# Kernel optimization log

Measured on AMD Instinct MI355X. Metric: run time of the kernel, lower is better.

Reference implementation:

```python
import jax, jax.numpy as jnp
import numpy as np

EPS = 1e-5
GROUPS = 32


def _groupnorm(x, gamma, beta):
    B, C, H, W = x.shape
    xr = x.reshape(B, GROUPS, C // GROUPS, H, W)
    mu = xr.mean(axis=(2, 3, 4), keepdims=True)
    var = xr.var(axis=(2, 3, 4), keepdims=True)
    xn = ((xr - mu) * jax.lax.rsqrt(var + EPS)).reshape(B, C, H, W)
    return xn * gamma[None, :, None, None] + beta[None, :, None, None]


def _conv1x1(x, w, b):
    # x: [B,C,H,W], w: [Cout,Cin], b: [Cout]
    return jnp.einsum('bchw,oc->bohw', x, w) + b[None, :, None, None]


def setup_inputs() -> dict:
    key = jax.random.key(0)
    ks = jax.random.split(key, 11)
    B, C, H, W = 4, 64, 64, 64
    s = 0.05  # weight scale for well-conditioned softmax
    inp = {
        'x': jax.random.normal(ks[0], (B, C, H, W), jnp.float32),
        'gn_gamma': jnp.ones((C,), jnp.float32),
        'gn_beta': jnp.zeros((C,), jnp.float32),
        'wq': jax.random.normal(ks[1], (C, C), jnp.float32) * s,
        'bq': jnp.zeros((C,), jnp.float32),
        'wk': jax.random.normal(ks[2], (C, C), jnp.float32) * s,
        'bk': jnp.zeros((C,), jnp.float32),
        'wv': jax.random.normal(ks[3], (C, C), jnp.float32) * s,
        'bv': jnp.zeros((C,), jnp.float32),
        'wp': jax.random.normal(ks[4], (C, C), jnp.float32) * s,
        'bp': jnp.zeros((C,), jnp.float32),
    }
    return inp


def reference(x, gn_gamma, gn_beta, wq, bq, wk, bk, wv, bv, wp, bp):
    B, C, H, W = x.shape
    h = _groupnorm(x, gn_gamma, gn_beta)
    q = _conv1x1(h, wq, bq)
    k = _conv1x1(h, wk, bk)
    v = _conv1x1(h, wv, bv)
    # scores over all spatial positions: [B,H,W,H,W]
    scale = 1.0 / jnp.sqrt(jnp.asarray(C, x.dtype))
    w = jnp.einsum('bchw,bcHW->bhwHW', q, k) * scale
    w = jax.nn.softmax(w.reshape(B, H, W, H * W), axis=-1).reshape(B, H, W, H, W)
    h = jnp.einsum('bhwHW,bcHW->bchw', w, v)
    h = _conv1x1(h, wp, bp)
    return x + h
```

## Files before the change

### kernel.cpp

```cpp
#include <hip/hip_runtime.h>
#include <stdint.h>

#define Bn 4
#define Cn 64
#define Sn 4096
#define Gn 32

typedef float v4f __attribute__((ext_vector_type(4)));
typedef short v8s __attribute__((ext_vector_type(8)));
typedef short v4s __attribute__((ext_vector_type(4)));

#define MFMA16(a,b,c) __builtin_amdgcn_mfma_f32_16x16x32_bf16((a),(b),(c),0,0,0)

__device__ __forceinline__ float bf2f(uint16_t u){
  union { uint32_t i; float f; } x; x.i = ((uint32_t)u) << 16; return x.f;
}
__device__ __forceinline__ uint16_t f2bf(float f){
  union { float f; uint32_t i; } x; x.f = f;
  uint32_t r = x.i + 0x7fffu + ((x.i >> 16) & 1u);
  return (uint16_t)(r >> 16);
}
__device__ __forceinline__ uint32_t cvtpk(float a, float b){
  uint32_t r;
  asm("v_cvt_pk_bf16_f32 %0, %1, %2" : "=v"(r) : "v"(a), "v"(b));
  return r;
}
__device__ __forceinline__ v8s pack8(float4 a, float4 b){
  v8s r;
  r[0]=(short)f2bf(a.x); r[1]=(short)f2bf(a.y); r[2]=(short)f2bf(a.z); r[3]=(short)f2bf(a.w);
  r[4]=(short)f2bf(b.x); r[5]=(short)f2bf(b.y); r[6]=(short)f2bf(b.z); r[7]=(short)f2bf(b.w);
  return r;
}

__global__ __launch_bounds__(256) void gn_stats(const float* __restrict__ x,
                                                float* __restrict__ stats)
{
  const int tid = threadIdx.x;
  const float* base = x + (size_t)blockIdx.x * 8192;
  float sum = 0.f, sq = 0.f;
  #pragma unroll
  for (int i = 0; i < 8; ++i) {
    float4 v = *(const float4*)(base + ((i << 8) + tid)*4);
    sum += v.x + v.y + v.z + v.w;
    sq  += v.x*v.x + v.y*v.y + v.z*v.z + v.w*v.w;
  }
  #pragma unroll
  for (int off = 1; off < 64; off <<= 1) {
    sum += __shfl_xor(sum, off);
    sq  += __shfl_xor(sq, off);
  }
  __shared__ float red[8];
  const int w = tid >> 6;
  if ((tid & 63) == 0) { red[w] = sum; red[4+w] = sq; }
  __syncthreads();
  if (tid == 0) {
    float s = red[0]+red[1]+red[2]+red[3];
    float q = red[4]+red[5]+red[6]+red[7];
    float mean = s * (1.f/8192.f);
    float var  = q * (1.f/8192.f) - mean*mean;
    stats[blockIdx.x]       = mean;
    stats[128 + blockIdx.x] = rsqrtf(fmaxf(var, 0.f) + 1e-5f);
  }
}

__global__ __launch_bounds__(256) void gn_qkv(
    const float* __restrict__ xg, const float* __restrict__ gamma,
    const float* __restrict__ beta,
    const float* __restrict__ wq, const float* __restrict__ bq,
    const float* __restrict__ wk, const float* __restrict__ bk,
    const float* __restrict__ wv, const float* __restrict__ bv,
    const float* __restrict__ stats,
    uint16_t* __restrict__ Qg, uint16_t* __restrict__ Kg, uint16_t* __restrict__ Vg)
{
  __shared__ uint16_t Hs[16*72];
  const int tid  = threadIdx.x;
  const int w    = tid >> 6;
  const int lane = tid & 63;
  const int l15  = lane & 15;
  const int quad = lane >> 4;
  const int b      = blockIdx.x >> 8;
  const int s_base = (blockIdx.x & 255) << 4;
  const float QSC = 0.18033688011112042f;

  {
    const int c = lane;
    const int g = c >> 1;
    const float mean = stats[b*Gn + g];
    const float rstd = stats[128 + b*Gn + g];
    const float ga = gamma[c], be = beta[c];
    float4 v = *(const float4*)(xg + ((size_t)b*Cn + c)*Sn + s_base + (w << 2));
    const int r0 = w << 2;
    Hs[(r0+0)*72 + c] = f2bf((v.x - mean)*rstd*ga + be);
    Hs[(r0+1)*72 + c] = f2bf((v.y - mean)*rstd*ga + be);
    Hs[(r0+2)*72 + c] = f2bf((v.z - mean)*rstd*ga + be);
    Hs[(r0+3)*72 + c] = f2bf((v.w - mean)*rstd*ga + be);
  }
  __syncthreads();

  v8s bh0 = *(const v8s*)(Hs + l15*72 + (quad << 3));
  v8s bh1 = *(const v8s*)(Hs + l15*72 + 32 + (quad << 3));

  #pragma unroll
  for (int t = 0; t < 3; ++t) {
    const int ot   = w*3 + t;
    const int wsel = ot >> 2;
    const int o16  = (ot & 3) << 4;
    const float* Wsel = (wsel == 0) ? wq : (wsel == 1) ? wk : wv;
    const float* Bsel = (wsel == 0) ? bq : (wsel == 1) ? bk : bv;
    const float* Wr = Wsel + (o16 + l15)*64 + (quad << 3);
    v8s a0 = pack8(*(const float4*)(Wr),      *(const float4*)(Wr + 4));
    v8s a1 = pack8(*(const float4*)(Wr + 32), *(const float4*)(Wr + 36));
    v4f d = (v4f){0.f,0.f,0.f,0.f};
    d = MFMA16(a0, bh0, d);
    d = MFMA16(a1, bh1, d);
    const int s = s_base + l15;
    if (wsel <= 1) {
      v4s qv;
      #pragma unroll
      for (int r = 0; r < 4; ++r) {
        float val = d[r] + Bsel[o16 + (quad << 2) + r];
        if (wsel == 0) val *= QSC;
        qv[r] = (short)f2bf(val);
      }
      uint16_t* dst = (wsel == 0 ? Qg : Kg) + ((size_t)b*Sn + s)*64 + o16 + (quad << 2);
      *(v4s*)dst = qv;
    } else {
      #pragma unroll
      for (int r = 0; r < 4; ++r) {
        const int o = o16 + (quad << 2) + r;
        Vg[((size_t)b*Cn + o)*Sn + s] = f2bf(d[r] + Bsel[o]);
      }
    }
  }
}

__global__ __launch_bounds__(256) void attn_split(
    const uint16_t* __restrict__ Qg, const uint16_t* __restrict__ Kg,
    const uint16_t* __restrict__ Vg,
    uint16_t* __restrict__ Opart, float* __restrict__ lpart)
{
  __shared__ uint16_t Ks[2][64*72];
  __shared__ uint16_t Vs[2][64*72];

  const int tid  = threadIdx.x;
  const int w    = tid >> 6;
  const int lane = tid & 63;
  const int l15  = lane & 15;
  const int quad = lane >> 4;
  const int bx    = blockIdx.x;
  const int split = bx & 3;
  const int qt    = (bx >> 2) & 31;
  const int b     = bx >> 7;
  const int i_base = qt << 7;
  const int j0     = split << 10;

  const uint16_t* Qb = Qg + ((size_t)b*Sn + i_base)*64;
  const uint16_t* Kb = Kg + (size_t)b*Sn*64;
  const uint16_t* Vb = Vg + (size_t)b*Cn*Sn;

  v8s qb[2][2];
  #pragma unroll
  for (int h = 0; h < 2; ++h) {
    const int row = (w << 5) + (h << 4) + l15;
    qb[h][0] = *(const v8s*)(Qb + row*64 + (quad << 3));
    qb[h][1] = *(const v8s*)(Qb + row*64 + 32 + (quad << 3));
  }

  const int e0 = tid << 3,         r0 = e0 >> 6, c0 = e0 & 63;
  const int e1 = (256 + tid) << 3, r1 = e1 >> 6, c1 = e1 & 63;

  *(v8s*)(Ks[0] + r0*72 + c0) = *(const v8s*)(Kb + j0*64 + e0);
  *(v8s*)(Ks[0] + r1*72 + c1) = *(const v8s*)(Kb + j0*64 + e1);
  *(v8s*)(Vs[0] + r0*72 + c0) = *(const v8s*)(Vb + (size_t)r0*Sn + j0 + c0);
  *(v8s*)(Vs[0] + r1*72 + c1) = *(const v8s*)(Vb + (size_t)r1*Sn + j0 + c1);

  float lsum[2] = {0.f, 0.f};
  v4f o_acc[2][4];
  #pragma unroll
  for (int h = 0; h < 2; ++h)
    #pragma unroll
    for (int nc = 0; nc < 4; ++nc) o_acc[h][nc] = (v4f){0.f,0.f,0.f,0.f};

  __syncthreads();

  for (int kt = 0; kt < 16; ++kt) {
    const int cur = kt & 1;
    v8s kp0, kp1, vp0, vp1;
    if (kt < 15) {
      const int jb = j0 + ((kt + 1) << 6);
      kp0 = *(const v8s*)(Kb + jb*64 + e0);
      kp1 = *(const v8s*)(Kb + jb*64 + e1);
      vp0 = *(const v8s*)(Vb + (size_t)r0*Sn + jb + c0);
      vp1 = *(const v8s*)(Vb + (size_t)r1*Sn + jb + c1);
    }

    v8s ka[4][2];
    #pragma unroll
    for (int n = 0; n < 4; ++n) {
      const uint16_t* kr = Ks[cur] + ((n << 4) + l15)*72;
      ka[n][0] = *(const v8s*)(kr + (quad << 3));
      ka[n][1] = *(const v8s*)(kr + 32 + (quad << 3));
    }

    v8s pa[2][2];
    #pragma unroll
    for (int h = 0; h < 2; ++h) {
      v4f s[4];
      #pragma unroll
      for (int n = 0; n < 4; ++n) {
        v4f t = (v4f){0.f,0.f,0.f,0.f};
        t = MFMA16(ka[n][0], qb[h][0], t);
        t = MFMA16(ka[n][1], qb[h][1], t);
        s[n] = t;
      }
      union { v8s s8; uint32_t u[4]; } u0, u1;
      #pragma unroll
      for (int n = 0; n < 4; ++n) {
        const float p0 = __builtin_amdgcn_exp2f(s[n][0]);
        const float p1 = __builtin_amdgcn_exp2f(s[n][1]);
        const float p2 = __builtin_amdgcn_exp2f(s[n][2]);
        const float p3 = __builtin_amdgcn_exp2f(s[n][3]);
        lsum[h] += (p0 + p1) + (p2 + p3);
        const uint32_t w0 = cvtpk(p0, p1);
        const uint32_t w1 = cvtpk(p2, p3);
        if (n < 2) { u0.u[(n & 1)*2] = w0; u0.u[(n & 1)*2 + 1] = w1; }
        else       { u1.u[(n & 1)*2] = w0; u1.u[(n & 1)*2 + 1] = w1; }
      }
      pa[h][0] = u0.s8;
      pa[h][1] = u1.s8;
    }

    #pragma unroll
    for (int nc = 0; nc < 4; ++nc) {
      const uint16_t* vrow = Vs[cur] + ((nc << 4) + l15)*72;
      #pragma unroll
      for (int c = 0; c < 2; ++c) {
        union { v8s s8; v4s h4[2]; } vb;
        vb.h4[0] = *(const v4s*)(vrow + (c << 5) + (quad << 2));
        vb.h4[1] = *(const v4s*)(vrow + (c << 5) + 16 + (quad << 2));
        o_acc[0][nc] = MFMA16(pa[0][c], vb.s8, o_acc[0][nc]);
        o_acc[1][nc] = MFMA16(pa[1][c], vb.s8, o_acc[1][nc]);
      }
    }

    if (kt < 15) {
      const int nxt = cur ^ 1;
      *(v8s*)(Ks[nxt] + r0*72 + c0) = kp0;
      *(v8s*)(Ks[nxt] + r1*72 + c1) = kp1;
      *(v8s*)(Vs[nxt] + r0*72 + c0) = vp0;
      *(v8s*)(Vs[nxt] + r1*72 + c1) = vp1;
      __syncthreads();
    }
  }

  #pragma unroll
  for (int h = 0; h < 2; ++h) {
    lsum[h] += __shfl_xor(lsum[h], 16);
    lsum[h] += __shfl_xor(lsum[h], 32);
  }

  uint16_t* Ob = Opart + (size_t)bx*8192 + (size_t)(w << 5)*64;
  float*    lp = lpart + bx*128 + (w << 5);
  #pragma unroll
  for (int h = 0; h < 2; ++h)
    #pragma unroll
    for (int nc = 0; nc < 4; ++nc)
      #pragma unroll
      for (int r = 0; r < 4; ++r)
        Ob[((h << 4) + (quad << 2) + r)*64 + (nc << 4) + l15] = f2bf(o_acc[h][nc][r]);
  if (lane < 16) {
    lp[l15]      = lsum[0];
    lp[16 + l15] = lsum[1];
  }
}

__global__ __launch_bounds__(256) void proj_res(
    const uint16_t* __restrict__ Opart, const float* __restrict__ lpart,
    const float* __restrict__ wp, const float* __restrict__ bp,
    const float* __restrict__ xg, float* __restrict__ out)
{
  __shared__ uint16_t As[16*72];
  const int tid  = threadIdx.x;
  const int w    = tid >> 6;
  const int lane = tid & 63;
  const int l15  = lane & 15;
  const int quad = lane >> 4;
  const int b      = blockIdx.x >> 8;
  const int st     = blockIdx.x & 255;
  const int qt     = st >> 3;
  const int sub    = st & 7;
  const int s_base = st << 4;

  const uint16_t* po = Opart + (size_t)((b*32 + qt)*4)*8192 + (sub << 4)*64;
  const float*    pl = lpart + ((b*32 + qt)*4)*128 + (sub << 4);

  {
    const int e = tid << 2, row = tid >> 4, col = (tid & 15) << 2;
    const float linv = 1.f / (pl[row] + pl[128+row] + pl[256+row] + pl[384+row]);
    float acc[4] = {0.f,0.f,0.f,0.f};
    #pragma unroll
    for (int sp = 0; sp < 4; ++sp) {
      v4s o = *(const v4s*)(po + (size_t)sp*8192 + e);
      #pragma unroll
      for (int j = 0; j < 4; ++j) acc[j] += bf2f((uint16_t)o[j]);
    }
    v4s a;
    #pragma unroll
    for (int j = 0; j < 4; ++j) a[j] = (short)f2bf(acc[j]*linv);
    *(v4s*)(As + row*72 + col) = a;
  }
  __syncthreads();

  v8s ba0 = *(const v8s*)(As + l15*72 + (quad << 3));
  v8s ba1 = *(const v8s*)(As + l15*72 + 32 + (quad << 3));

  const float* Wr = wp + ((w << 4) + l15)*64 + (quad << 3);
  v8s a0 = pack8(*(const float4*)(Wr),      *(const float4*)(Wr + 4));
  v8s a1 = pack8(*(const float4*)(Wr + 32), *(const float4*)(Wr + 36));
  v4f d = (v4f){0.f,0.f,0.f,0.f};
  d = MFMA16(a0, ba0, d);
  d = MFMA16(a1, ba1, d);
  const int s = s_base + l15;
  #pragma unroll
  for (int r = 0; r < 4; ++r) {
    const int o = (w << 4) + (quad << 2) + r;
    const size_t idx = ((size_t)b*Cn + o)*Sn + s;
    out[idx] = d[r] + bp[o] + xg[idx];
  }
}

extern "C" void kernel_launch(void* const* d_in, const int* in_sizes, int n_in,
                              void* d_out, int out_size, void* d_ws, size_t ws_size,
                              hipStream_t stream)
{
  const float* x     = (const float*)d_in[0];
  const float* gamma = (const float*)d_in[1];
  const float* beta  = (const float*)d_in[2];
  const float* wq    = (const float*)d_in[3];
  const float* bq    = (const float*)d_in[4];
  const float* wk    = (const float*)d_in[5];
  const float* bk    = (const float*)d_in[6];
  const float* wv    = (const float*)d_in[7];
  const float* bv    = (const float*)d_in[8];
  const float* wp    = (const float*)d_in[9];
  const float* bp    = (const float*)d_in[10];

  float*    stats = (float*)d_ws;
  uint16_t* Qg    = (uint16_t*)d_ws + 1024;
  uint16_t* Kg    = Qg + (size_t)Bn*Sn*Cn;
  uint16_t* Vg    = Kg + (size_t)Bn*Sn*Cn;
  uint16_t* Opart = Vg + (size_t)Bn*Sn*Cn;
  float*    lpart = (float*)(Opart + (size_t)512*8192);
  float*    outp  = (float*)d_out;

  gn_stats  <<<128, 256, 0, stream>>>(x, stats);
  gn_qkv    <<<1024, 256, 0, stream>>>(x, gamma, beta, wq, bq, wk, bk, wv, bv,
                                       stats, Qg, Kg, Vg);
  attn_split<<<512, 256, 0, stream>>>(Qg, Kg, Vg, Opart, lpart);
  proj_res  <<<1024, 256, 0, stream>>>(Opart, lpart, wp, bp, x, outp);
}
```

Baseline: 120.0 us.

## Split attention keys eightfly, compute row sums via MFMA, pre-convert weights to bf16

```diff
diff --git a/kernel.cpp b/kernel.cpp
--- a/kernel.cpp
+++ b/kernel.cpp
@@ -12,6 +12,8 @@
 
 #define MFMA16(a,b,c) __builtin_amdgcn_mfma_f32_16x16x32_bf16((a),(b),(c),0,0,0)
 
+#define QSC 0.18033688011112042f
+
 __device__ __forceinline__ float bf2f(uint16_t u){
   union { uint32_t i; float f; } x; x.i = ((uint32_t)u) << 16; return x.f;
 }
@@ -25,17 +27,30 @@
   asm("v_cvt_pk_bf16_f32 %0, %1, %2" : "=v"(r) : "v"(a), "v"(b));
   return r;
 }
-__device__ __forceinline__ v8s pack8(float4 a, float4 b){
-  v8s r;
-  r[0]=(short)f2bf(a.x); r[1]=(short)f2bf(a.y); r[2]=(short)f2bf(a.z); r[3]=(short)f2bf(a.w);
-  r[4]=(short)f2bf(b.x); r[5]=(short)f2bf(b.y); r[6]=(short)f2bf(b.z); r[7]=(short)f2bf(b.w);
-  return r;
-}
-
-__global__ __launch_bounds__(256) void gn_stats(const float* __restrict__ x,
-                                                float* __restrict__ stats)
+
+__global__ __launch_bounds__(256) void gn_stats(
+    const float* __restrict__ x,
+    const float* __restrict__ wq, const float* __restrict__ wk,
+    const float* __restrict__ wv, const float* __restrict__ wp,
+    float* __restrict__ stats, uint16_t* __restrict__ Wbf)
 {
   const int tid = threadIdx.x;
+  if (blockIdx.x >= 128) {
+    const int m = blockIdx.x - 128;
+    const float* src = (m == 0) ? wq : (m == 1) ? wk : (m == 2) ? wv : wp;
+    const float sc  = (m == 0) ? QSC : 1.f;
+    uint16_t* dst = Wbf + (m << 12);
+    #pragma unroll
+    for (int i = 0; i < 4; ++i) {
+      const int e = (tid << 4) + (i << 2);
+      float4 v = *(const float4*)(src + e);
+      v4s o;
+      o[0] = (short)f2bf(v.x*sc); o[1] = (short)f2bf(v.y*sc);
+      o[2] = (short)f2bf(v.z*sc); o[3] = (short)f2bf(v.w*sc);
+      *(v4s*)(dst + e) = o;
+    }
+    return;
+  }
   const float* base = x + (size_t)blockIdx.x * 8192;
   float sum = 0.f, sq = 0.f;
   #pragma unroll
@@ -65,10 +80,9 @@
 
 __global__ __launch_bounds__(256) void gn_qkv(
     const float* __restrict__ xg, const float* __restrict__ gamma,
-    const float* __restrict__ beta,
-    const float* __restrict__ wq, const float* __restrict__ bq,
-    const float* __restrict__ wk, const float* __restrict__ bk,
-    const float* __restrict__ wv, const float* __restrict__ bv,
+    const float* __restrict__ beta, const uint16_t* __restrict__ Wbf,
+    const float* __restrict__ bq, const float* __restrict__ bk,
+    const float* __restrict__ bv,
     const float* __restrict__ stats,
     uint16_t* __restrict__ Qg, uint16_t* __restrict__ Kg, uint16_t* __restrict__ Vg)
 {
@@ -80,7 +94,6 @@
   const int quad = lane >> 4;
   const int b      = blockIdx.x >> 8;
   const int s_base = (blockIdx.x & 255) << 4;
-  const float QSC = 0.18033688011112042f;
 
   {
     const int c = lane;
@@ -105,11 +118,11 @@
     const int ot   = w*3 + t;
     const int wsel = ot >> 2;
     const int o16  = (ot & 3) << 4;
-    const float* Wsel = (wsel == 0) ? wq : (wsel == 1) ? wk : wv;
     const float* Bsel = (wsel == 0) ? bq : (wsel == 1) ? bk : bv;
-    const float* Wr = Wsel + (o16 + l15)*64 + (quad << 3);
-    v8s a0 = pack8(*(const float4*)(Wr),      *(const float4*)(Wr + 4));
-    v8s a1 = pack8(*(const float4*)(Wr + 32), *(const float4*)(Wr + 36));
+    const float bsc   = (wsel == 0) ? QSC : 1.f;
+    const uint16_t* Wr = Wbf + (wsel << 12) + (o16 + l15)*64 + (quad << 3);
+    v8s a0 = *(const v8s*)(Wr);
+    v8s a1 = *(const v8s*)(Wr + 32);
     v4f d = (v4f){0.f,0.f,0.f,0.f};
     d = MFMA16(a0, bh0, d);
     d = MFMA16(a1, bh1, d);
@@ -117,11 +130,8 @@
     if (wsel <= 1) {
       v4s qv;
       #pragma unroll
-      for (int r = 0; r < 4; ++r) {
-        float val = d[r] + Bsel[o16 + (quad << 2) + r];
-        if (wsel == 0) val *= QSC;
-        qv[r] = (short)f2bf(val);
-      }
+      for (int r = 0; r < 4; ++r)
+        qv[r] = (short)f2bf(d[r] + Bsel[o16 + (quad << 2) + r]*bsc);
       uint16_t* dst = (wsel == 0 ? Qg : Kg) + ((size_t)b*Sn + s)*64 + o16 + (quad << 2);
       *(v4s*)dst = qv;
     } else {
@@ -134,7 +144,7 @@
   }
 }
 
-__global__ __launch_bounds__(256) void attn_split(
+__global__ __launch_bounds__(256, 4) void attn_split(
     const uint16_t* __restrict__ Qg, const uint16_t* __restrict__ Kg,
     const uint16_t* __restrict__ Vg,
     uint16_t* __restrict__ Opart, float* __restrict__ lpart)
@@ -148,11 +158,11 @@
   const int l15  = lane & 15;
   const int quad = lane >> 4;
   const int bx    = blockIdx.x;
-  const int split = bx & 3;
-  const int qt    = (bx >> 2) & 31;
-  const int b     = bx >> 7;
+  const int split = bx & 7;
+  const int qt    = (bx >> 3) & 31;
+  const int b     = bx >> 8;
   const int i_base = qt << 7;
-  const int j0     = split << 10;
+  const int j0     = split << 9;
 
   const uint16_t* Qb = Qg + ((size_t)b*Sn + i_base)*64;
   const uint16_t* Kb = Kg + (size_t)b*Sn*64;
@@ -174,19 +184,23 @@
   *(v8s*)(Vs[0] + r0*72 + c0) = *(const v8s*)(Vb + (size_t)r0*Sn + j0 + c0);
   *(v8s*)(Vs[0] + r1*72 + c1) = *(const v8s*)(Vb + (size_t)r1*Sn + j0 + c1);
 
-  float lsum[2] = {0.f, 0.f};
+  const v8s ones8 = (v8s){0x3F80,0x3F80,0x3F80,0x3F80,0x3F80,0x3F80,0x3F80,0x3F80};
+
+  v4f o_l[2];
   v4f o_acc[2][4];
   #pragma unroll
-  for (int h = 0; h < 2; ++h)
+  for (int h = 0; h < 2; ++h) {
+    o_l[h] = (v4f){0.f,0.f,0.f,0.f};
     #pragma unroll
     for (int nc = 0; nc < 4; ++nc) o_acc[h][nc] = (v4f){0.f,0.f,0.f,0.f};
+  }
 
   __syncthreads();
 
-  for (int kt = 0; kt < 16; ++kt) {
+  for (int kt = 0; kt < 8; ++kt) {
     const int cur = kt & 1;
     v8s kp0, kp1, vp0, vp1;
-    if (kt < 15) {
+    if (kt < 7) {
       const int jb = j0 + ((kt + 1) << 6);
       kp0 = *(const v8s*)(Kb + jb*64 + e0);
       kp1 = *(const v8s*)(Kb + jb*64 + e1);
@@ -220,7 +234,6 @@
         const float p1 = __builtin_amdgcn_exp2f(s[n][1]);
         const float p2 = __builtin_amdgcn_exp2f(s[n][2]);
         const float p3 = __builtin_amdgcn_exp2f(s[n][3]);
-        lsum[h] += (p0 + p1) + (p2 + p3);
         const uint32_t w0 = cvtpk(p0, p1);
         const uint32_t w1 = cvtpk(p2, p3);
         if (n < 2) { u0.u[(n & 1)*2] = w0; u0.u[(n & 1)*2 + 1] = w1; }
@@ -228,6 +241,8 @@
       }
       pa[h][0] = u0.s8;
       pa[h][1] = u1.s8;
+      o_l[h] = MFMA16(pa[h][0], ones8, o_l[h]);
+      o_l[h] = MFMA16(pa[h][1], ones8, o_l[h]);
     }
 
     #pragma unroll
@@ -243,7 +258,7 @@
       }
     }
 
-    if (kt < 15) {
+    if (kt < 7) {
       const int nxt = cur ^ 1;
       *(v8s*)(Ks[nxt] + r0*72 + c0) = kp0;
       *(v8s*)(Ks[nxt] + r1*72 + c1) = kp1;
@@ -253,12 +268,6 @@
     }
   }
 
-  #pragma unroll
-  for (int h = 0; h < 2; ++h) {
-    lsum[h] += __shfl_xor(lsum[h], 16);
-    lsum[h] += __shfl_xor(lsum[h], 32);
-  }
-
   uint16_t* Ob = Opart + (size_t)bx*8192 + (size_t)(w << 5)*64;
   float*    lp = lpart + bx*128 + (w << 5);
   #pragma unroll
@@ -268,15 +277,18 @@
       #pragma unroll
       for (int r = 0; r < 4; ++r)
         Ob[((h << 4) + (quad << 2) + r)*64 + (nc << 4) + l15] = f2bf(o_acc[h][nc][r]);
-  if (lane < 16) {
-    lp[l15]      = lsum[0];
-    lp[16 + l15] = lsum[1];
+  if (l15 == 0) {
+    #pragma unroll
+    for (int h = 0; h < 2; ++h)
+      #pragma unroll
+      for (int r = 0; r < 4; ++r)
+        lp[(h << 4) + (quad << 2) + r] = o_l[h][r];
   }
 }
 
 __global__ __launch_bounds__(256) void proj_res(
     const uint16_t* __restrict__ Opart, const float* __restrict__ lpart,
-    const float* __restrict__ wp, const float* __restrict__ bp,
+    const uint16_t* __restrict__ Wbf, const float* __restrict__ bp,
     const float* __restrict__ xg, float* __restrict__ out)
 {
   __shared__ uint16_t As[16*72];
@@ -291,15 +303,18 @@
   const int sub    = st & 7;
   const int s_base = st << 4;
 
-  const uint16_t* po = Opart + (size_t)((b*32 + qt)*4)*8192 + (sub << 4)*64;
-  const float*    pl = lpart + ((b*32 + qt)*4)*128 + (sub << 4);
+  const uint16_t* po = Opart + (size_t)((b*32 + qt)*8)*8192 + (sub << 4)*64;
+  const float*    pl = lpart + ((b*32 + qt)*8)*128 + (sub << 4);
 
   {
     const int e = tid << 2, row = tid >> 4, col = (tid & 15) << 2;
-    const float linv = 1.f / (pl[row] + pl[128+row] + pl[256+row] + pl[384+row]);
+    float lsum = 0.f;
+    #pragma unroll
+    for (int sp = 0; sp < 8; ++sp) lsum += pl[sp*128 + row];
+    const float linv = 1.f / lsum;
     float acc[4] = {0.f,0.f,0.f,0.f};
     #pragma unroll
-    for (int sp = 0; sp < 4; ++sp) {
+    for (int sp = 0; sp < 8; ++sp) {
       v4s o = *(const v4s*)(po + (size_t)sp*8192 + e);
       #pragma unroll
       for (int j = 0; j < 4; ++j) acc[j] += bf2f((uint16_t)o[j]);
@@ -314,9 +329,9 @@
   v8s ba0 = *(const v8s*)(As + l15*72 + (quad << 3));
   v8s ba1 = *(const v8s*)(As + l15*72 + 32 + (quad << 3));
 
-  const float* Wr = wp + ((w << 4) + l15)*64 + (quad << 3);
-  v8s a0 = pack8(*(const float4*)(Wr),      *(const float4*)(Wr + 4));
-  v8s a1 = pack8(*(const float4*)(Wr + 32), *(const float4*)(Wr + 36));
+  const uint16_t* Wr = Wbf + (3 << 12) + ((w << 4) + l15)*64 + (quad << 3);
+  v8s a0 = *(const v8s*)(Wr);
+  v8s a1 = *(const v8s*)(Wr + 32);
   v4f d = (v4f){0.f,0.f,0.f,0.f};
   d = MFMA16(a0, ba0, d);
   d = MFMA16(a1, ba1, d);
@@ -346,16 +361,17 @@
   const float* bp    = (const float*)d_in[10];
 
   float*    stats = (float*)d_ws;
-  uint16_t* Qg    = (uint16_t*)d_ws + 1024;
+  uint16_t* Wbf   = (uint16_t*)d_ws + 2048;
+  uint16_t* Qg    = (uint16_t*)d_ws + 32768;
   uint16_t* Kg    = Qg + (size_t)Bn*Sn*Cn;
   uint16_t* Vg    = Kg + (size_t)Bn*Sn*Cn;
   uint16_t* Opart = Vg + (size_t)Bn*Sn*Cn;
-  float*    lpart = (float*)(Opart + (size_t)512*8192);
+  float*    lpart = (float*)(Opart + (size_t)1024*8192);
   float*    outp  = (float*)d_out;
 
-  gn_stats  <<<128, 256, 0, stream>>>(x, stats);
-  gn_qkv    <<<1024, 256, 0, stream>>>(x, gamma, beta, wq, bq, wk, bk, wv, bv,
+  gn_stats  <<<132, 256, 0, stream>>>(x, wq, wk, wv, wp, stats, Wbf);
+  gn_qkv    <<<1024, 256, 0, stream>>>(x, gamma, beta, Wbf, bq, bk, bv,
                                        stats, Qg, Kg, Vg);
-  attn_split<<<512, 256, 0, stream>>>(Qg, Kg, Vg, Opart, lpart);
-  proj_res  <<<1024, 256, 0, stream>>>(Opart, lpart, wp, bp, x, outp);
-}
+  attn_split<<<1024, 256, 0, stream>>>(Qg, Kg, Vg, Opart, lpart);
+  proj_res  <<<1024, 256, 0, stream>>>(Opart, lpart, Wbf, bp, x, outp);
+}
```

Measured after the change: 113.6 us. 5.3% less time.
